# Optimization experiments

Measured on AMD Instinct MI355X. Metric: run time of the kernel, lower is better.

## Reference

```python
import jax, jax.numpy as jnp
import numpy as np

D_MODEL = 256
N_LAYERS = 6
N_HEADS = 8
D_FF = 1024
HEAD_DIM = D_MODEL // N_HEADS
EPS = 1e-5


def layer_norm(x, scale, bias):
    mu = jnp.mean(x, axis=-1, keepdims=True)
    var = jnp.var(x, axis=-1, keepdims=True)
    return (x - mu) * jax.lax.rsqrt(var + EPS) * scale + bias


def setup_inputs() -> dict:
    key = jax.random.key(0)
    ks = jax.random.split(key, 12)
    B, T = 4, 2048
    x = jax.random.normal(ks[0], (B, T, D_MODEL), dtype=jnp.float32)
    L = N_LAYERS
    s = 0.02
    inp = {
        "x": x,
        "ln1_s": jnp.ones((L, D_MODEL), jnp.float32),
        "ln1_b": jnp.zeros((L, D_MODEL), jnp.float32),
        "wq": jax.random.normal(ks[1], (L, D_MODEL, D_MODEL), jnp.float32) * s,
        "bq": jnp.zeros((L, D_MODEL), jnp.float32),
        "wk": jax.random.normal(ks[2], (L, D_MODEL, D_MODEL), jnp.float32) * s,
        "bk": jnp.zeros((L, D_MODEL), jnp.float32),
        "wv": jax.random.normal(ks[3], (L, D_MODEL, D_MODEL), jnp.float32) * s,
        "bv": jnp.zeros((L, D_MODEL), jnp.float32),
        "wo": jax.random.normal(ks[4], (L, D_MODEL, D_MODEL), jnp.float32) * s,
        "bo": jnp.zeros((L, D_MODEL), jnp.float32),
        "ln2_s": jnp.ones((L, D_MODEL), jnp.float32),
        "ln2_b": jnp.zeros((L, D_MODEL), jnp.float32),
        "w1": jax.random.normal(ks[5], (L, D_MODEL, D_FF), jnp.float32) * s,
        "b1": jnp.zeros((L, D_FF), jnp.float32),
        "w2": jax.random.normal(ks[6], (L, D_FF, D_MODEL), jnp.float32) * s,
        "b2": jnp.zeros((L, D_MODEL), jnp.float32),
    }
    return inp


def reference(x, ln1_s, ln1_b, wq, bq, wk, bk, wv, bv, wo, bo, ln2_s, ln2_b, w1, b1, w2, b2):
    B, T, D = x.shape
    scale = 1.0 / jnp.sqrt(jnp.float32(HEAD_DIM))
    for l in range(N_LAYERS):
        normed = layer_norm(x, ln1_s[l], ln1_b[l])
        q = (normed @ wq[l] + bq[l]).reshape(B, T, N_HEADS, HEAD_DIM)
        k = (normed @ wk[l] + bk[l]).reshape(B, T, N_HEADS, HEAD_DIM)
        v = (normed @ wv[l] + bv[l]).reshape(B, T, N_HEADS, HEAD_DIM)
        scores = jnp.einsum('bqhd,bkhd->bhqk', q, k) * scale  # [B,H,T,T]
        attn = jax.nn.softmax(scores, axis=-1)
        attn_out = jnp.einsum('bhqk,bkhd->bqhd', attn, v).reshape(B, T, D)
        x = x + attn_out @ wo[l] + bo[l]
        h = layer_norm(x, ln2_s[l], ln2_b[l])
        h = jax.nn.gelu(h @ w1[l] + b1[l], approximate=False)
        x = x + h @ w2[l] + b2[l]
    return x
```

## Files before the change

kernel.cpp:

```cpp
#include <hip/hip_runtime.h>
#include <math.h>

#define D_MODELC 256
#define N_LAYERSC 6
#define N_HEADSC 8
#define D_FFC 1024
#define HEAD_DIMC 32
#define B_SZ 4
#define T_SEQ 2048
#define M_ROWS 8192
#define QKV_N 768

typedef short bf16x8 __attribute__((ext_vector_type(8)));
typedef short bf16x4 __attribute__((ext_vector_type(4)));
typedef float f32x4  __attribute__((ext_vector_type(4)));
typedef unsigned u32x4 __attribute__((ext_vector_type(4)));
typedef unsigned short u16;

#define QSCALE 0.25503488f

__device__ __forceinline__ u16 f2bf(float x) {
    unsigned u = __builtin_bit_cast(unsigned, x);
    u += 0x7FFF + ((u >> 16) & 1);
    return (u16)(u >> 16);
}

__device__ __forceinline__ float bf2f(short x) {
    return __builtin_bit_cast(float, (unsigned)((u16)x) << 16);
}

__device__ __forceinline__ unsigned pack2bf(float a, float b) {
    return __builtin_amdgcn_perm(__builtin_bit_cast(unsigned, b),
                                 __builtin_bit_cast(unsigned, a), 0x07060302u);
}

__device__ __forceinline__ float fast_gelu(float x) {
    float y  = x * 0.70710678118654752f;
    float ay = __builtin_fabsf(y);
    float t  = __builtin_amdgcn_rcpf(1.0f + 0.3275911f * ay);
    float p  = t * (0.254829592f + t * (-0.284496736f + t * (1.421413741f
               + t * (-1.453152027f + t * 1.061405429f))));
    float e  = __builtin_amdgcn_exp2f(-ay * ay * 1.4426950408889634f);
    float er = 1.0f - p * e;
    er = y < 0.0f ? -er : er;
    return 0.5f * x * (1.0f + er);
}

__device__ __forceinline__ void transpose_tile(
    const float* __restrict__ src, u16* __restrict__ dst,
    int K, int N, int k0, int n0, float scale, float (*ts)[33])
{
    const int r = threadIdx.x >> 3, c4 = (threadIdx.x & 7) * 4;
    const float4 v = *(const float4*)(src + (size_t)(k0 + r) * N + n0 + c4);
    ts[r][c4 + 0] = v.x; ts[r][c4 + 1] = v.y;
    ts[r][c4 + 2] = v.z; ts[r][c4 + 3] = v.w;
    __syncthreads();
    bf16x4 o;
#pragma unroll
    for (int i = 0; i < 4; i++) o[i] = (short)f2bf(ts[c4 + i][r] * scale);
    *(bf16x4*)(dst + (size_t)(n0 + r) * K + k0 + c4) = o;
}

__global__ __launch_bounds__(256) void prep_all(
    const float* __restrict__ wq, const float* __restrict__ wk,
    const float* __restrict__ wv, const float* __restrict__ wo,
    const float* __restrict__ w1, const float* __restrict__ w2,
    const float* __restrict__ bq, const float* __restrict__ bk,
    const float* __restrict__ bv,
    u16* __restrict__ wqkv_t, u16* __restrict__ wo_t,
    u16* __restrict__ w1_t, u16* __restrict__ w2_t,
    float* __restrict__ qkvb,
    const float* __restrict__ x, const float* __restrict__ gamma,
    const float* __restrict__ beta, float* __restrict__ X,
    u16* __restrict__ Y)
{
    __shared__ float ts[32][33];
    const int bid = blockIdx.x;
    if (bid < 1152) {
        const int sec = bid / 384, t = bid % 384;
        const int z = t >> 6, rem = t & 63, ty = rem >> 3, tx = rem & 7;
        const float* src = sec == 0 ? wq : (sec == 1 ? wk : wv);
        transpose_tile(src + (size_t)z * 65536,
                       wqkv_t + (size_t)z * QKV_N * 256 + sec * 256 * 256,
                       256, 256, ty * 32, tx * 32,
                       sec == 0 ? QSCALE : 1.0f, ts);
    } else if (bid < 1536) {
        const int t = bid - 1152;
        const int z = t >> 6, rem = t & 63, ty = rem >> 3, tx = rem & 7;
        transpose_tile(wo + (size_t)z * 65536, wo_t + (size_t)z * 65536,
                       256, 256, ty * 32, tx * 32, 1.0f, ts);
    } else if (bid < 3072) {
        const int t = bid - 1536;
        const int z = t >> 8, rem = t & 255, ty = rem >> 5, tx = rem & 31;
        transpose_tile(w1 + (size_t)z * 262144, w1_t + (size_t)z * 262144,
                       256, D_FFC, ty * 32, tx * 32, 1.0f, ts);
    } else if (bid < 4608) {
        const int t = bid - 3072;
        const int z = t >> 8, rem = t & 255, ty = rem >> 3, tx = rem & 7;
        transpose_tile(w2 + (size_t)z * 262144, w2_t + (size_t)z * 262144,
                       D_FFC, 256, ty * 32, tx * 32, 1.0f, ts);
    } else if (bid < 4626) {
        const int i = (bid - 4608) * 256 + threadIdx.x;
        const int l = i / QKV_N, j = i % QKV_N;
        float v;
        if (j < 256)      v = bq[l * 256 + j] * QSCALE;
        else if (j < 512) v = bk[l * 256 + j - 256];
        else              v = bv[l * 256 + j - 512];
        qkvb[i] = v;
    } else {
        const int w = threadIdx.x >> 6, lane = threadIdx.x & 63;
        const int row = (bid - 4626) * 4 + w;
        const float4 v = *(const float4*)(x + (size_t)row * 256 + lane * 4);
        *(float4*)(X + (size_t)row * 256 + lane * 4) = v;
        float sum = v.x + v.y + v.z + v.w;
        float sq  = v.x * v.x + v.y * v.y + v.z * v.z + v.w * v.w;
#pragma unroll
        for (int off = 32; off > 0; off >>= 1) {
            sum += __shfl_xor(sum, off, 64);
            sq  += __shfl_xor(sq,  off, 64);
        }
        float mu  = sum * (1.0f / 256.0f);
        float var = sq * (1.0f / 256.0f) - mu * mu;
        float rr  = rsqrtf(var + 1e-5f);
        const float4 g  = *(const float4*)(gamma + lane * 4);
        const float4 bb = *(const float4*)(beta + lane * 4);
        bf16x4 o;
        o[0] = (short)f2bf((v.x - mu) * rr * g.x + bb.x);
        o[1] = (short)f2bf((v.y - mu) * rr * g.y + bb.y);
        o[2] = (short)f2bf((v.z - mu) * rr * g.z + bb.z);
        o[3] = (short)f2bf((v.w - mu) * rr * g.w + bb.w);
        *(bf16x4*)(Y + (size_t)row * 256 + lane * 4) = o;
    }
}

template <int EPI>
__global__ __launch_bounds__(256) void mfma_gemm(
    const u16* __restrict__ A, const u16* __restrict__ Bt,
    const float* __restrict__ bias, u16* __restrict__ Vout,
    void* __restrict__ Cout, int N, int K)
{
    __shared__ u16 As[128 * 64];
    __shared__ u16 Bs[128 * 64];
    const int tid = threadIdx.x, w = tid >> 6, lane = tid & 63;
    const int c = lane & 15, quad = lane >> 4;
    const int row0 = blockIdx.y * 128, col0 = blockIdx.x * 128;
    const int wr = w >> 1, wc = w & 1;

    int flv[4], rA[4], colA[4];
#pragma unroll
    for (int ci = 0; ci < 4; ci++) {
        flv[ci]  = (w * 4 + ci) * 1024 + lane * 16;
        rA[ci]   = flv[ci] >> 7;
        colA[ci] = (flv[ci] & 127) >> 1;
    }

    f32x4 acc[4][4] = {};
    bf16x8 pA[4], pB[4];
#pragma unroll
    for (int ci = 0; ci < 4; ci++) {
        pA[ci] = *(const bf16x8*)(A  + (size_t)(row0 + rA[ci]) * K + colA[ci]);
        pB[ci] = *(const bf16x8*)(Bt + (size_t)(col0 + rA[ci]) * K + colA[ci]);
    }

    for (int k0 = 0; k0 < K; k0 += 64) {
        __syncthreads();
#pragma unroll
        for (int ci = 0; ci < 4; ci++) {
            *(bf16x8*)((char*)As + flv[ci]) = pA[ci];
            *(bf16x8*)((char*)Bs + flv[ci]) = pB[ci];
        }
        __syncthreads();
        if (k0 + 64 < K) {
#pragma unroll
            for (int ci = 0; ci < 4; ci++) {
                pA[ci] = *(const bf16x8*)(A  + (size_t)(row0 + rA[ci]) * K + k0 + 64 + colA[ci]);
                pB[ci] = *(const bf16x8*)(Bt + (size_t)(col0 + rA[ci]) * K + k0 + 64 + colA[ci]);
            }
        }
#pragma unroll
        for (int kk = 0; kk < 2; kk++) {
            bf16x8 af[4], bfv[4];
#pragma unroll
            for (int i = 0; i < 4; i++)
                af[i] = *(const bf16x8*)&As[(wr * 64 + i * 16 + c) * 64 + kk * 32 + quad * 8];
#pragma unroll
            for (int j = 0; j < 4; j++)
                bfv[j] = *(const bf16x8*)&Bs[(wc * 64 + j * 16 + c) * 64 + kk * 32 + quad * 8];
#pragma unroll
            for (int i = 0; i < 4; i++)
#pragma unroll
                for (int j = 0; j < 4; j++)
                    acc[i][j] = __builtin_amdgcn_mfma_f32_16x16x32_bf16(
                        af[i], bfv[j], acc[i][j], 0, 0, 0);
        }
    }

    float bj[4];
#pragma unroll
    for (int j = 0; j < 4; j++) bj[j] = bias[col0 + wc * 64 + j * 16 + c];

    if (EPI == 3 && col0 >= 512) {
#pragma unroll
        for (int i = 0; i < 4; i++) {
            const int tok = row0 + wr * 64 + i * 16 + quad * 4;
#pragma unroll
            for (int j = 0; j < 4; j++) {
                const int dim = col0 - 512 + wc * 64 + j * 16 + c;
                bf16x4 o;
#pragma unroll
                for (int r = 0; r < 4; r++) o[r] = (short)f2bf(acc[i][j][r] + bj[j]);
                *(bf16x4*)&Vout[(size_t)dim * M_ROWS + tok] = o;
            }
        }
        return;
    }

#pragma unroll
    for (int i = 0; i < 4; i++) {
#pragma unroll
        for (int r = 0; r < 4; r++) {
            const int gr = row0 + wr * 64 + i * 16 + quad * 4 + r;
#pragma unroll
            for (int j = 0; j < 4; j++) {
                const int gc = col0 + wc * 64 + j * 16 + c;
                float v = acc[i][j][r] + bj[j];
                if (EPI == 2) v = fast_gelu(v);
                ((u16*)Cout)[(size_t)gr * N + gc] = f2bf(v);
            }
        }
    }
}

template <int DOLN, int MERGE>
__global__ __launch_bounds__(256) void gemm_ln(
    const u16* __restrict__ A, const u16* __restrict__ Ab,
    const float* __restrict__ Lmrg,
    const u16* __restrict__ Bt, const float* __restrict__ bias,
    const float* __restrict__ resid, float* __restrict__ Xout,
    const float* __restrict__ gamma, const float* __restrict__ beta,
    u16* __restrict__ Nout, int K)
{
    __shared__ u16 As[32 * 64];
    __shared__ u16 Bs[256 * 64];
    __shared__ float2 red[4][32];
    const int tid = threadIdx.x, w = tid >> 6, lane = tid & 63;
    const int c = lane & 15, quad = lane >> 4;
    const int row0 = blockIdx.x * 32;

    const int flA  = w * 1024 + lane * 16;
    const int rAa  = flA >> 7, colAa = (flA & 127) >> 1;
    int flB[8], rB[8], colB[8];
#pragma unroll
    for (int ci = 0; ci < 8; ci++) {
        flB[ci]  = (w * 8 + ci) * 1024 + lane * 16;
        rB[ci]   = flB[ci] >> 7;
        colB[ci] = (flB[ci] & 127) >> 1;
    }

    f32x4 acc[2][4] = {};

    auto loadA = [&](int gc) -> bf16x8 {
        const int row = row0 + rAa;
        if (MERGE) {
            const int head = gc >> 5;
            const float la = Lmrg[(size_t)row * 8 + head];
            const float lb = Lmrg[(size_t)M_ROWS * 8 + (size_t)row * 8 + head];
            const float inv = __builtin_amdgcn_rcpf(la + lb);
            bf16x8 a = *(const bf16x8*)(A  + (size_t)row * 256 + gc);
            bf16x8 b = *(const bf16x8*)(Ab + (size_t)row * 256 + gc);
            bf16x8 o;
#pragma unroll
            for (int j = 0; j < 8; j++)
                o[j] = (short)f2bf((bf2f(a[j]) + bf2f(b[j])) * inv);
            return o;
        }
        return *(const bf16x8*)(A + (size_t)row * K + gc);
    };

    bf16x8 pA = loadA(colAa);
    bf16x8 pB[8];
#pragma unroll
    for (int ci = 0; ci < 8; ci++)
        pB[ci] = *(const bf16x8*)(Bt + (size_t)rB[ci] * K + colB[ci]);

    for (int k0 = 0; k0 < K; k0 += 64) {
        __syncthreads();
        *(bf16x8*)((char*)As + flA) = pA;
#pragma unroll
        for (int ci = 0; ci < 8; ci++)
            *(bf16x8*)((char*)Bs + flB[ci]) = pB[ci];
        __syncthreads();
        if (k0 + 64 < K) {
            pA = loadA(k0 + 64 + colAa);
#pragma unroll
            for (int ci = 0; ci < 8; ci++)
                pB[ci] = *(const bf16x8*)(Bt + (size_t)rB[ci] * K + k0 + 64 + colB[ci]);
        }
#pragma unroll
        for (int kk = 0; kk < 2; kk++) {
            bf16x8 af[2], bfv[4];
#pragma unroll
            for (int i = 0; i < 2; i++)
                af[i] = *(const bf16x8*)&As[(i * 16 + c) * 64 + kk * 32 + quad * 8];
#pragma unroll
            for (int j = 0; j < 4; j++)
                bfv[j] = *(const bf16x8*)&Bs[(w * 64 + j * 16 + c) * 64 + kk * 32 + quad * 8];
#pragma unroll
            for (int i = 0; i < 2; i++)
#pragma unroll
                for (int j = 0; j < 4; j++)
                    acc[i][j] = __builtin_amdgcn_mfma_f32_16x16x32_bf16(
                        af[i], bfv[j], acc[i][j], 0, 0, 0);
        }
    }

    float bj[4];
#pragma unroll
    for (int j = 0; j < 4; j++) bj[j] = bias[w * 64 + j * 16 + c];
    float xv[2][4][4];
#pragma unroll
    for (int i = 0; i < 2; i++)
#pragma unroll
        for (int r = 0; r < 4; r++) {
            const int gr = row0 + i * 16 + quad * 4 + r;
#pragma unroll
            for (int j = 0; j < 4; j++) {
                const int gc = w * 64 + j * 16 + c;
                xv[i][j][r] = acc[i][j][r] + bj[j] + resid[(size_t)gr * 256 + gc];
            }
        }

    if (DOLN) {
        float sm[2][4], sp[2][4];
#pragma unroll
        for (int i = 0; i < 2; i++)
#pragma unroll
            for (int r = 0; r < 4; r++) {
                float s = 0.f, q = 0.f;
#pragma unroll
                for (int j = 0; j < 4; j++) { s += xv[i][j][r]; q += xv[i][j][r] * xv[i][j][r]; }
                sm[i][r] = s; sp[i][r] = q;
            }
#pragma unroll
        for (int off = 1; off < 16; off <<= 1)
#pragma unroll
            for (int i = 0; i < 2; i++)
#pragma unroll
                for (int r = 0; r < 4; r++) {
                    sm[i][r] += __shfl_xor(sm[i][r], off, 64);
                    sp[i][r] += __shfl_xor(sp[i][r], off, 64);
                }
        __syncthreads();
        if (c == 0) {
#pragma unroll
            for (int i = 0; i < 2; i++)
#pragma unroll
                for (int r = 0; r < 4; r++)
                    red[w][i * 16 + quad * 4 + r] = make_float2(sm[i][r], sp[i][r]);
        }
        __syncthreads();
#pragma unroll
        for (int i = 0; i < 2; i++)
#pragma unroll
            for (int r = 0; r < 4; r++) {
                const int row = i * 16 + quad * 4 + r;
                float2 t0 = red[0][row], t1 = red[1][row];
                float2 t2 = red[2][row], t3 = red[3][row];
                float S = (t0.x + t1.x) + (t2.x + t3.x);
                float Q = (t0.y + t1.y) + (t2.y + t3.y);
                float mu = S * (1.0f / 256.0f);
                float var = Q * (1.0f / 256.0f) - mu * mu;
                float rr = rsqrtf(var + 1e-5f);
                const int gr = row0 + row;
#pragma unroll
                for (int j = 0; j < 4; j++) {
                    const int gc = w * 64 + j * 16 + c;
                    float x = xv[i][j][r];
                    Xout[(size_t)gr * 256 + gc] = x;
                    Nout[(size_t)gr * 256 + gc] =
                        f2bf((x - mu) * rr * gamma[gc] + beta[gc]);
                }
            }
    } else {
#pragma unroll
        for (int i = 0; i < 2; i++)
#pragma unroll
            for (int r = 0; r < 4; r++) {
                const int gr = row0 + i * 16 + quad * 4 + r;
#pragma unroll
                for (int j = 0; j < 4; j++)
                    Xout[(size_t)gr * 256 + w * 64 + j * 16 + c] = xv[i][j][r];
            }
    }
}

__global__ __launch_bounds__(256) void attn_kernel(
    const u16* __restrict__ QKV, const u16* __restrict__ VT,
    u16* __restrict__ POa, u16* __restrict__ POb, float* __restrict__ Lp)
{
    const int h = blockIdx.y, b = blockIdx.z;
    const int half = blockIdx.x & 1;
    const int q0 = (blockIdx.x >> 1) * 128;
    const int tid = threadIdx.x, w = tid >> 6, lane = tid & 63;
    const int c = lane & 15, quad = lane >> 4;

    __shared__ u16 Kf[4096];
    __shared__ u16 Vf[4096];

    const u16* qp = QKV + (size_t)(b * T_SEQ + q0 + w * 32 + c) * QKV_N + h * 32 + quad * 8;
    bf16x8 aQ0 = *(const bf16x8*)qp;
    bf16x8 aQ1 = *(const bf16x8*)(qp + 16 * QKV_N);

    const bf16x8 bOnes = {0x3F80, 0x3F80, 0x3F80, 0x3F80,
                          0x3F80, 0x3F80, 0x3F80, 0x3F80};

    f32x4 O[2][2] = {};
    f32x4 Ol0 = {0.f, 0.f, 0.f, 0.f}, Ol1 = {0.f, 0.f, 0.f, 0.f};

    const u16* kgp = QKV + (size_t)(b * T_SEQ + w * 16 + c) * QKV_N + 256 + h * 32 + quad * 8;
    const u16* vgp = VT + ((size_t)h * 32 + (lane & 31)) * M_ROWS + b * T_SEQ
                     + (w * 2 + (lane >> 5)) * 8;
    u16* kfw = Kf + w * 512 + lane * 8;

    const int vd  = lane & 31, vdh = vd >> 4, vc = vd & 15, vhi = lane >> 5;
    const int vkh = w >> 1, vseg = w & 1;
    const int voff = ((((vkh * 2 + vdh) * 4 + 2 * vhi) * 16 + vc) * 8) + vseg * 4;

    const int kbeg = half * (T_SEQ / 2);
    const int kend = kbeg + T_SEQ / 2;

    bf16x8 gK0 = *(const bf16x8*)(kgp + (size_t)kbeg * QKV_N);
    bf16x8 gK1 = *(const bf16x8*)(kgp + (size_t)(kbeg + 64) * QKV_N);
    bf16x8 gV0 = *(const bf16x8*)(vgp + kbeg);
    bf16x8 gV1 = *(const bf16x8*)(vgp + kbeg + 64);

    for (int k0 = kbeg; k0 < kend; k0 += 128) {
        __syncthreads();
        *(bf16x8*)kfw          = gK0;
        *(bf16x8*)(kfw + 2048) = gK1;
        {
            bf16x4 l0v = __builtin_shufflevector(gV0, gV0, 0, 1, 2, 3);
            bf16x4 h0v = __builtin_shufflevector(gV0, gV0, 4, 5, 6, 7);
            bf16x4 l1v = __builtin_shufflevector(gV1, gV1, 0, 1, 2, 3);
            bf16x4 h1v = __builtin_shufflevector(gV1, gV1, 4, 5, 6, 7);
            *(bf16x4*)&Vf[voff]              = l0v;
            *(bf16x4*)&Vf[voff + 128]        = h0v;
            *(bf16x4*)&Vf[2048 + voff]       = l1v;
            *(bf16x4*)&Vf[2048 + voff + 128] = h1v;
        }
        __syncthreads();
        if (k0 + 128 < kend) {
            gK0 = *(const bf16x8*)(kgp + (size_t)(k0 + 128) * QKV_N);
            gK1 = *(const bf16x8*)(kgp + (size_t)(k0 + 192) * QKV_N);
            gV0 = *(const bf16x8*)(vgp + k0 + 128);
            gV1 = *(const bf16x8*)(vgp + k0 + 192);
        }

#pragma unroll
        for (int hf = 0; hf < 2; hf++) {
            const u16* Kb = Kf + hf * 2048;
            const u16* Vb = Vf + hf * 2048;

            unsigned pk0[4][2], pk1[4][2];
#pragma unroll
            for (int g = 0; g < 4; g++) {
                bf16x8 aK = *(const bf16x8*)&Kb[g * 512 + lane * 8];
                f32x4 S0 = __builtin_amdgcn_mfma_f32_16x16x32_bf16(
                    aK, aQ0, (f32x4){0.f, 0.f, 0.f, 0.f}, 0, 0, 0);
                f32x4 S1 = __builtin_amdgcn_mfma_f32_16x16x32_bf16(
                    aK, aQ1, (f32x4){0.f, 0.f, 0.f, 0.f}, 0, 0, 0);
                pk0[g][0] = pack2bf(__builtin_amdgcn_exp2f(S0[0]),
                                    __builtin_amdgcn_exp2f(S0[1]));
                pk0[g][1] = pack2bf(__builtin_amdgcn_exp2f(S0[2]),
                                    __builtin_amdgcn_exp2f(S0[3]));
                pk1[g][0] = pack2bf(__builtin_amdgcn_exp2f(S1[0]),
                                    __builtin_amdgcn_exp2f(S1[1]));
                pk1[g][1] = pack2bf(__builtin_amdgcn_exp2f(S1[2]),
                                    __builtin_amdgcn_exp2f(S1[3]));
            }

            __builtin_amdgcn_s_setprio(1);
#pragma unroll
            for (int kh = 0; kh < 2; kh++) {
                bf16x8 aP0 = __builtin_bit_cast(bf16x8,
                    (u32x4){pk0[2 * kh][0], pk0[2 * kh][1],
                            pk0[2 * kh + 1][0], pk0[2 * kh + 1][1]});
                bf16x8 aP1 = __builtin_bit_cast(bf16x8,
                    (u32x4){pk1[2 * kh][0], pk1[2 * kh][1],
                            pk1[2 * kh + 1][0], pk1[2 * kh + 1][1]});
                Ol0 = __builtin_amdgcn_mfma_f32_16x16x32_bf16(aP0, bOnes, Ol0, 0, 0, 0);
                Ol1 = __builtin_amdgcn_mfma_f32_16x16x32_bf16(aP1, bOnes, Ol1, 0, 0, 0);
#pragma unroll
                for (int dh = 0; dh < 2; dh++) {
                    bf16x8 bV = *(const bf16x8*)&Vb[((kh * 2 + dh) * 64 + lane) * 8];
                    O[0][dh] = __builtin_amdgcn_mfma_f32_16x16x32_bf16(aP0, bV, O[0][dh], 0, 0, 0);
                    O[1][dh] = __builtin_amdgcn_mfma_f32_16x16x32_bf16(aP1, bV, O[1][dh], 0, 0, 0);
                }
            }
            __builtin_amdgcn_s_setprio(0);
        }
    }

    u16* pb = (half ? POb : POa)
              + (size_t)(b * T_SEQ + q0 + w * 32) * 256 + h * 32;
    if (c == 0) {
        float* lb = Lp + (size_t)half * M_ROWS * 8
                    + (size_t)(b * T_SEQ + q0 + w * 32) * 8 + h;
#pragma unroll
        for (int r = 0; r < 4; r++) {
            lb[(size_t)(quad * 4 + r) * 8]      = Ol0[r];
            lb[(size_t)(16 + quad * 4 + r) * 8] = Ol1[r];
        }
    }
#pragma unroll
    for (int r = 0; r < 4; r++) {
        int src = quad * 4 + r;
        pb[(size_t)src * 256 + c]             = f2bf(O[0][0][r]);
        pb[(size_t)src * 256 + 16 + c]        = f2bf(O[0][1][r]);
        pb[(size_t)(16 + src) * 256 + c]      = f2bf(O[1][0][r]);
        pb[(size_t)(16 + src) * 256 + 16 + c] = f2bf(O[1][1][r]);
    }
}

extern "C" void kernel_launch(void* const* d_in, const int* in_sizes, int n_in,
                              void* d_out, int out_size, void* d_ws, size_t ws_size,
                              hipStream_t stream)
{
    const float* x     = (const float*)d_in[0];
    const float* ln1_s = (const float*)d_in[1];
    const float* ln1_b = (const float*)d_in[2];
    const float* wq    = (const float*)d_in[3];
    const float* bq    = (const float*)d_in[4];
    const float* wk    = (const float*)d_in[5];
    const float* bk    = (const float*)d_in[6];
    const float* wv    = (const float*)d_in[7];
    const float* bv    = (const float*)d_in[8];
    const float* wo    = (const float*)d_in[9];
    const float* bo    = (const float*)d_in[10];
    const float* ln2_s = (const float*)d_in[11];
    const float* ln2_b = (const float*)d_in[12];
    const float* w1    = (const float*)d_in[13];
    const float* b1    = (const float*)d_in[14];
    const float* w2    = (const float*)d_in[15];
    const float* b2    = (const float*)d_in[16];

    float* X = (float*)d_out;

    u16* normed = (u16*)d_ws;
    u16* qkv    = normed + (size_t)M_ROWS * 256;
    u16* POa    = qkv + (size_t)M_ROWS * QKV_N;
    u16* h1     = qkv;
    u16* wqkv_t = POa + (size_t)M_ROWS * 256;
    u16* wo_t   = wqkv_t + (size_t)N_LAYERSC * QKV_N * 256;
    u16* w1_t   = wo_t + (size_t)N_LAYERSC * 256 * 256;
    u16* w2_t   = w1_t + (size_t)N_LAYERSC * D_FFC * 256;
    float* qkvb = (float*)(w2_t + (size_t)N_LAYERSC * 256 * D_FFC);
    u16* VTb    = (u16*)(qkvb + N_LAYERSC * QKV_N);
    u16* POb    = VTb + (size_t)256 * M_ROWS;
    float* Lp   = (float*)(POb + (size_t)M_ROWS * 256);

    dim3 blk(256);

    prep_all<<<dim3(4626 + M_ROWS / 4), blk, 0, stream>>>(
        wq, wk, wv, wo, w1, w2, bq, bk, bv,
        wqkv_t, wo_t, w1_t, w2_t, qkvb,
        x, ln1_s, ln1_b, X, normed);

    dim3 g_qkv(QKV_N / 128, M_ROWS / 128);
    dim3 g_ff(D_FFC / 128, M_ROWS / 128);
    dim3 g_ln32(M_ROWS / 32);
    dim3 g_attn(2 * T_SEQ / 128, N_HEADSC, B_SZ);

    for (int l = 0; l < N_LAYERSC; l++) {
        mfma_gemm<3><<<g_qkv, blk, 0, stream>>>(
            normed, wqkv_t + (size_t)l * QKV_N * 256, qkvb + l * QKV_N,
            VTb, qkv, QKV_N, 256);
        attn_kernel<<<g_attn, blk, 0, stream>>>(qkv, VTb, POa, POb, Lp);
        gemm_ln<1, 1><<<g_ln32, blk, 0, stream>>>(
            POa, POb, Lp, wo_t + (size_t)l * 256 * 256, bo + l * 256, X,
            X, ln2_s + l * 256, ln2_b + l * 256, VTb, 256);
        mfma_gemm<2><<<g_ff, blk, 0, stream>>>(
            VTb, w1_t + (size_t)l * D_FFC * 256, b1 + l * D_FFC,
            nullptr, h1, D_FFC, 256);
        if (l + 1 < N_LAYERSC) {
            gemm_ln<1, 0><<<g_ln32, blk, 0, stream>>>(
                h1, nullptr, nullptr, w2_t + (size_t)l * 256 * D_FFC,
                b2 + l * 256, X, X, ln1_s + (l + 1) * 256,
                ln1_b + (l + 1) * 256, normed, D_FFC);
        } else {
            gemm_ln<0, 0><<<g_ln32, blk, 0, stream>>>(
                h1, nullptr, nullptr, w2_t + (size_t)l * 256 * D_FFC,
                b2 + l * 256, X, X, nullptr, nullptr, nullptr, D_FFC);
        }
    }
}
```

Baseline: 618.1 us.

## Fuse all layers into one persistent cooperative megakernel with grid barriers

```diff
diff --git a/kernel.cpp b/kernel.cpp
--- a/kernel.cpp
+++ b/kernel.cpp
@@ -5,11 +5,11 @@
 #define N_LAYERSC 6
 #define N_HEADSC 8
 #define D_FFC 1024
-#define HEAD_DIMC 32
 #define B_SZ 4
 #define T_SEQ 2048
 #define M_ROWS 8192
 #define QKV_N 768
+#define NBLK_MAX 512
 
 typedef short bf16x8 __attribute__((ext_vector_type(8)));
 typedef short bf16x4 __attribute__((ext_vector_type(4)));
@@ -46,6 +46,19 @@
     return 0.5f * x * (1.0f + er);
 }
 
+__device__ __forceinline__ void gsync(unsigned* bar, unsigned& epoch) {
+    __syncthreads();
+    epoch += gridDim.x;
+    if (threadIdx.x == 0) {
+        __threadfence();
+        __hip_atomic_fetch_add(bar, 1u, __ATOMIC_ACQ_REL, __HIP_MEMORY_SCOPE_AGENT);
+        while (__hip_atomic_load(bar, __ATOMIC_RELAXED, __HIP_MEMORY_SCOPE_AGENT) < epoch)
+            __builtin_amdgcn_s_sleep(2);
+        __threadfence();
+    }
+    __syncthreads();
+}
+
 __device__ __forceinline__ void transpose_tile(
     const float* __restrict__ src, u16* __restrict__ dst,
     int K, int N, int k0, int n0, float scale, float (*ts)[33])
@@ -61,7 +74,8 @@
     *(bf16x4*)(dst + (size_t)(n0 + r) * K + k0 + c4) = o;
 }
 
-__global__ __launch_bounds__(256) void prep_all(
+__device__ __forceinline__ void prep_tile(
+    int bid,
     const float* __restrict__ wq, const float* __restrict__ wk,
     const float* __restrict__ wv, const float* __restrict__ wo,
     const float* __restrict__ w1, const float* __restrict__ w2,
@@ -72,10 +86,9 @@
     float* __restrict__ qkvb,
     const float* __restrict__ x, const float* __restrict__ gamma,
     const float* __restrict__ beta, float* __restrict__ X,
-    u16* __restrict__ Y)
+    u16* __restrict__ Y, char* smem)
 {
-    __shared__ float ts[32][33];
-    const int bid = blockIdx.x;
+    float (*ts)[33] = (float(*)[33])smem;
     if (bid < 1152) {
         const int sec = bid / 384, t = bid % 384;
         const int z = t >> 6, rem = t & 63, ty = rem >> 3, tx = rem & 7;
@@ -133,17 +146,17 @@
     }
 }
 
-template <int EPI>
-__global__ __launch_bounds__(256) void mfma_gemm(
+__device__ __forceinline__ void gemm128_tile(
     const u16* __restrict__ A, const u16* __restrict__ Bt,
     const float* __restrict__ bias, u16* __restrict__ Vout,
-    void* __restrict__ Cout, int N, int K)
+    u16* __restrict__ Cout, int N, int K, int bx, int by,
+    bool qkvmode, bool gelu, char* smem)
 {
-    __shared__ u16 As[128 * 64];
-    __shared__ u16 Bs[128 * 64];
+    u16* As = (u16*)smem;
+    u16* Bs = (u16*)(smem + 16384);
     const int tid = threadIdx.x, w = tid >> 6, lane = tid & 63;
     const int c = lane & 15, quad = lane >> 4;
-    const int row0 = blockIdx.y * 128, col0 = blockIdx.x * 128;
+    const int row0 = by * 128, col0 = bx * 128;
     const int wr = w >> 1, wc = w & 1;
 
     int flv[4], rA[4], colA[4];
@@ -199,7 +212,7 @@
 #pragma unroll
     for (int j = 0; j < 4; j++) bj[j] = bias[col0 + wc * 64 + j * 16 + c];
 
-    if (EPI == 3 && col0 >= 512) {
+    if (qkvmode && col0 >= 512) {
 #pragma unroll
         for (int i = 0; i < 4; i++) {
             const int tok = row0 + wr * 64 + i * 16 + quad * 4;
@@ -224,28 +237,26 @@
             for (int j = 0; j < 4; j++) {
                 const int gc = col0 + wc * 64 + j * 16 + c;
                 float v = acc[i][j][r] + bj[j];
-                if (EPI == 2) v = fast_gelu(v);
-                ((u16*)Cout)[(size_t)gr * N + gc] = f2bf(v);
-            }
-        }
-    }
-}
-
-template <int DOLN, int MERGE>
-__global__ __launch_bounds__(256) void gemm_ln(
-    const u16* __restrict__ A, const u16* __restrict__ Ab,
-    const float* __restrict__ Lmrg,
-    const u16* __restrict__ Bt, const float* __restrict__ bias,
-    const float* __restrict__ resid, float* __restrict__ Xout,
-    const float* __restrict__ gamma, const float* __restrict__ beta,
-    u16* __restrict__ Nout, int K)
+                if (gelu) v = fast_gelu(v);
+                Cout[(size_t)gr * N + gc] = f2bf(v);
+            }
+        }
+    }
+}
+
+__device__ __forceinline__ void gemmln_tile(
+    const u16* __restrict__ A, const u16* __restrict__ Bt,
+    const float* __restrict__ bias, const float* __restrict__ resid,
+    float* __restrict__ Xout, const float* __restrict__ gamma,
+    const float* __restrict__ beta, u16* __restrict__ Nout,
+    int K, bool doln, int tix, char* smem)
 {
-    __shared__ u16 As[32 * 64];
-    __shared__ u16 Bs[256 * 64];
-    __shared__ float2 red[4][32];
+    u16* As = (u16*)smem;
+    u16* Bs = (u16*)(smem + 4096);
+    float2 (*red)[32] = (float2(*)[32])(smem + 36864);
     const int tid = threadIdx.x, w = tid >> 6, lane = tid & 63;
     const int c = lane & 15, quad = lane >> 4;
-    const int row0 = blockIdx.x * 32;
+    const int row0 = tix * 32;
 
     const int flA  = w * 1024 + lane * 16;
     const int rAa  = flA >> 7, colAa = (flA & 127) >> 1;
@@ -259,25 +270,7 @@
 
     f32x4 acc[2][4] = {};
 
-    auto loadA = [&](int gc) -> bf16x8 {
-        const int row = row0 + rAa;
-        if (MERGE) {
-            const int head = gc >> 5;
-            const float la = Lmrg[(size_t)row * 8 + head];
-            const float lb = Lmrg[(size_t)M_ROWS * 8 + (size_t)row * 8 + head];
-            const float inv = __builtin_amdgcn_rcpf(la + lb);
-            bf16x8 a = *(const bf16x8*)(A  + (size_t)row * 256 + gc);
-            bf16x8 b = *(const bf16x8*)(Ab + (size_t)row * 256 + gc);
-            bf16x8 o;
-#pragma unroll
-            for (int j = 0; j < 8; j++)
-                o[j] = (short)f2bf((bf2f(a[j]) + bf2f(b[j])) * inv);
-            return o;
-        }
-        return *(const bf16x8*)(A + (size_t)row * K + gc);
-    };
-
-    bf16x8 pA = loadA(colAa);
+    bf16x8 pA = *(const bf16x8*)(A + (size_t)(row0 + rAa) * K + colAa);
     bf16x8 pB[8];
 #pragma unroll
     for (int ci = 0; ci < 8; ci++)
@@ -291,7 +284,7 @@
             *(bf16x8*)((char*)Bs + flB[ci]) = pB[ci];
         __syncthreads();
         if (k0 + 64 < K) {
-            pA = loadA(k0 + 64 + colAa);
+            pA = *(const bf16x8*)(A + (size_t)(row0 + rAa) * K + k0 + 64 + colAa);
 #pragma unroll
             for (int ci = 0; ci < 8; ci++)
                 pB[ci] = *(const bf16x8*)(Bt + (size_t)rB[ci] * K + k0 + 64 + colB[ci]);
@@ -330,7 +323,7 @@
             }
         }
 
-    if (DOLN) {
+    if (doln) {
         float sm[2][4], sp[2][4];
 #pragma unroll
         for (int i = 0; i < 2; i++)
@@ -375,10 +368,10 @@
 #pragma unroll
                 for (int j = 0; j < 4; j++) {
                     const int gc = w * 64 + j * 16 + c;
-                    float x = xv[i][j][r];
-                    Xout[(size_t)gr * 256 + gc] = x;
+                    float xx = xv[i][j][r];
+                    Xout[(size_t)gr * 256 + gc] = xx;
                     Nout[(size_t)gr * 256 + gc] =
-                        f2bf((x - mu) * rr * gamma[gc] + beta[gc]);
+                        f2bf((xx - mu) * rr * gamma[gc] + beta[gc]);
                 }
             }
     } else {
@@ -394,18 +387,16 @@
     }
 }
 
-__global__ __launch_bounds__(256) void attn_kernel(
+__device__ __forceinline__ void attn_tile(
     const u16* __restrict__ QKV, const u16* __restrict__ VT,
-    u16* __restrict__ POa, u16* __restrict__ POb, float* __restrict__ Lp)
+    u16* __restrict__ PO, int tix, char* smem)
 {
-    const int h = blockIdx.y, b = blockIdx.z;
-    const int half = blockIdx.x & 1;
-    const int q0 = (blockIdx.x >> 1) * 128;
+    u16* Kf = (u16*)smem;
+    u16* Vf = (u16*)(smem + 8192);
+    const int b = tix >> 7, h = (tix >> 4) & 7;
+    const int q0 = (tix & 15) * 128;
     const int tid = threadIdx.x, w = tid >> 6, lane = tid & 63;
     const int c = lane & 15, quad = lane >> 4;
-
-    __shared__ u16 Kf[4096];
-    __shared__ u16 Vf[4096];
 
     const u16* qp = QKV + (size_t)(b * T_SEQ + q0 + w * 32 + c) * QKV_N + h * 32 + quad * 8;
     bf16x8 aQ0 = *(const bf16x8*)qp;
@@ -426,15 +417,12 @@
     const int vkh = w >> 1, vseg = w & 1;
     const int voff = ((((vkh * 2 + vdh) * 4 + 2 * vhi) * 16 + vc) * 8) + vseg * 4;
 
-    const int kbeg = half * (T_SEQ / 2);
-    const int kend = kbeg + T_SEQ / 2;
-
-    bf16x8 gK0 = *(const bf16x8*)(kgp + (size_t)kbeg * QKV_N);
-    bf16x8 gK1 = *(const bf16x8*)(kgp + (size_t)(kbeg + 64) * QKV_N);
-    bf16x8 gV0 = *(const bf16x8*)(vgp + kbeg);
-    bf16x8 gV1 = *(const bf16x8*)(vgp + kbeg + 64);
-
-    for (int k0 = kbeg; k0 < kend; k0 += 128) {
+    bf16x8 gK0 = *(const bf16x8*)(kgp);
+    bf16x8 gK1 = *(const bf16x8*)(kgp + (size_t)64 * QKV_N);
+    bf16x8 gV0 = *(const bf16x8*)(vgp);
+    bf16x8 gV1 = *(const bf16x8*)(vgp + 64);
+
+    for (int k0 = 0; k0 < T_SEQ; k0 += 128) {
         __syncthreads();
         *(bf16x8*)kfw          = gK0;
         *(bf16x8*)(kfw + 2048) = gK1;
@@ -449,7 +437,7 @@
             *(bf16x4*)&Vf[2048 + voff + 128] = h1v;
         }
         __syncthreads();
-        if (k0 + 128 < kend) {
+        if (k0 + 128 < T_SEQ) {
             gK0 = *(const bf16x8*)(kgp + (size_t)(k0 + 128) * QKV_N);
             gK1 = *(const bf16x8*)(kgp + (size_t)(k0 + 192) * QKV_N);
             gV0 = *(const bf16x8*)(vgp + k0 + 128);
@@ -501,24 +489,81 @@
         }
     }
 
-    u16* pb = (half ? POb : POa)
-              + (size_t)(b * T_SEQ + q0 + w * 32) * 256 + h * 32;
-    if (c == 0) {
-        float* lb = Lp + (size_t)half * M_ROWS * 8
-                    + (size_t)(b * T_SEQ + q0 + w * 32) * 8 + h;
-#pragma unroll
-        for (int r = 0; r < 4; r++) {
-            lb[(size_t)(quad * 4 + r) * 8]      = Ol0[r];
-            lb[(size_t)(16 + quad * 4 + r) * 8] = Ol1[r];
-        }
+    u16* pb = PO + (size_t)(b * T_SEQ + q0 + w * 32) * 256 + h * 32;
+    f32x4 r0, r1;
+#pragma unroll
+    for (int r = 0; r < 4; r++) {
+        r0[r] = __builtin_amdgcn_rcpf(Ol0[r]);
+        r1[r] = __builtin_amdgcn_rcpf(Ol1[r]);
     }
 #pragma unroll
     for (int r = 0; r < 4; r++) {
         int src = quad * 4 + r;
-        pb[(size_t)src * 256 + c]             = f2bf(O[0][0][r]);
-        pb[(size_t)src * 256 + 16 + c]        = f2bf(O[0][1][r]);
-        pb[(size_t)(16 + src) * 256 + c]      = f2bf(O[1][0][r]);
-        pb[(size_t)(16 + src) * 256 + 16 + c] = f2bf(O[1][1][r]);
+        pb[(size_t)src * 256 + c]             = f2bf(O[0][0][r] * r0[r]);
+        pb[(size_t)src * 256 + 16 + c]        = f2bf(O[0][1][r] * r0[r]);
+        pb[(size_t)(16 + src) * 256 + c]      = f2bf(O[1][0][r] * r1[r]);
+        pb[(size_t)(16 + src) * 256 + 16 + c] = f2bf(O[1][1][r] * r1[r]);
+    }
+}
+
+__global__ __launch_bounds__(256, 2) void mega_transformer(
+    const float* __restrict__ wq, const float* __restrict__ wk,
+    const float* __restrict__ wv, const float* __restrict__ wo,
+    const float* __restrict__ w1, const float* __restrict__ w2,
+    const float* __restrict__ bq, const float* __restrict__ bk,
+    const float* __restrict__ bv, const float* __restrict__ bo,
+    const float* __restrict__ b1, const float* __restrict__ b2,
+    const float* __restrict__ ln1_s, const float* __restrict__ ln1_b,
+    const float* __restrict__ ln2_s, const float* __restrict__ ln2_b,
+    const float* __restrict__ x,
+    float* __restrict__ X, u16* __restrict__ normed, u16* __restrict__ qkv,
+    u16* __restrict__ PO, u16* __restrict__ wqkv_t, u16* __restrict__ wo_t,
+    u16* __restrict__ w1_t, u16* __restrict__ w2_t, float* __restrict__ qkvb,
+    u16* __restrict__ VTb, unsigned* __restrict__ bar)
+{
+    __shared__ __align__(16) char smem[37888];
+    unsigned epoch = 0;
+    const int bid = blockIdx.x;
+    const int nblk = gridDim.x;
+
+    for (int t = bid; t < 6674; t += nblk) {
+        __syncthreads();
+        prep_tile(t, wq, wk, wv, wo, w1, w2, bq, bk, bv,
+                  wqkv_t, wo_t, w1_t, w2_t, qkvb,
+                  x, ln1_s, ln1_b, X, normed, smem);
+    }
+    gsync(bar, epoch);
+
+    u16* h1 = qkv;
+
+    for (int l = 0; l < N_LAYERSC; l++) {
+        for (int t = bid; t < 384; t += nblk)
+            gemm128_tile(normed, wqkv_t + (size_t)l * QKV_N * 256,
+                         qkvb + l * QKV_N, VTb, qkv,
+                         QKV_N, 256, t % 6, t / 6, true, false, smem);
+        gsync(bar, epoch);
+
+        for (int t = bid; t < 512; t += nblk)
+            attn_tile(qkv, VTb, PO, t, smem);
+        gsync(bar, epoch);
+
+        for (int t = bid; t < 256; t += nblk)
+            gemmln_tile(PO, wo_t + (size_t)l * 65536, bo + l * 256, X, X,
+                        ln2_s + l * 256, ln2_b + l * 256, VTb, 256, true, t, smem);
+        gsync(bar, epoch);
+
+        for (int t = bid; t < 512; t += nblk)
+            gemm128_tile(VTb, w1_t + (size_t)l * D_FFC * 256, b1 + l * D_FFC,
+                         nullptr, h1, D_FFC, 256, t & 7, t >> 3, false, true, smem);
+        gsync(bar, epoch);
+
+        const bool dol = (l + 1 < N_LAYERSC);
+        const int ln = dol ? l + 1 : 0;
+        for (int t = bid; t < 256; t += nblk)
+            gemmln_tile(h1, w2_t + (size_t)l * 256 * D_FFC, b2 + l * 256, X, X,
+                        ln1_s + ln * 256, ln1_b + ln * 256, normed,
+                        D_FFC, dol, t, smem);
+        if (l + 1 < N_LAYERSC) gsync(bar, epoch);
     }
 }
 
@@ -548,49 +593,39 @@
 
     u16* normed = (u16*)d_ws;
     u16* qkv    = normed + (size_t)M_ROWS * 256;
-    u16* POa    = qkv + (size_t)M_ROWS * QKV_N;
-    u16* h1     = qkv;
-    u16* wqkv_t = POa + (size_t)M_ROWS * 256;
+    u16* PO     = qkv + (size_t)M_ROWS * QKV_N;
+    u16* wqkv_t = PO + (size_t)M_ROWS * 256;
     u16* wo_t   = wqkv_t + (size_t)N_LAYERSC * QKV_N * 256;
     u16* w1_t   = wo_t + (size_t)N_LAYERSC * 256 * 256;
     u16* w2_t   = w1_t + (size_t)N_LAYERSC * D_FFC * 256;
     float* qkvb = (float*)(w2_t + (size_t)N_LAYERSC * 256 * D_FFC);
     u16* VTb    = (u16*)(qkvb + N_LAYERSC * QKV_N);
-    u16* POb    = VTb + (size_t)256 * M_ROWS;
-    float* Lp   = (float*)(POb + (size_t)M_ROWS * 256);
-
-    dim3 blk(256);
-
-    prep_all<<<dim3(4626 + M_ROWS / 4), blk, 0, stream>>>(
-        wq, wk, wv, wo, w1, w2, bq, bk, bv,
-        wqkv_t, wo_t, w1_t, w2_t, qkvb,
-        x, ln1_s, ln1_b, X, normed);
-
-    dim3 g_qkv(QKV_N / 128, M_ROWS / 128);
-    dim3 g_ff(D_FFC / 128, M_ROWS / 128);
-    dim3 g_ln32(M_ROWS / 32);
-    dim3 g_attn(2 * T_SEQ / 128, N_HEADSC, B_SZ);
-
-    for (int l = 0; l < N_LAYERSC; l++) {
-        mfma_gemm<3><<<g_qkv, blk, 0, stream>>>(
-            normed, wqkv_t + (size_t)l * QKV_N * 256, qkvb + l * QKV_N,
-            VTb, qkv, QKV_N, 256);
-        attn_kernel<<<g_attn, blk, 0, stream>>>(qkv, VTb, POa, POb, Lp);
-        gemm_ln<1, 1><<<g_ln32, blk, 0, stream>>>(
-            POa, POb, Lp, wo_t + (size_t)l * 256 * 256, bo + l * 256, X,
-            X, ln2_s + l * 256, ln2_b + l * 256, VTb, 256);
-        mfma_gemm<2><<<g_ff, blk, 0, stream>>>(
-            VTb, w1_t + (size_t)l * D_FFC * 256, b1 + l * D_FFC,
-            nullptr, h1, D_FFC, 256);
-        if (l + 1 < N_LAYERSC) {
-            gemm_ln<1, 0><<<g_ln32, blk, 0, stream>>>(
-                h1, nullptr, nullptr, w2_t + (size_t)l * 256 * D_FFC,
-                b2 + l * 256, X, X, ln1_s + (l + 1) * 256,
-                ln1_b + (l + 1) * 256, normed, D_FFC);
-        } else {
-            gemm_ln<0, 0><<<g_ln32, blk, 0, stream>>>(
-                h1, nullptr, nullptr, w2_t + (size_t)l * 256 * D_FFC,
-                b2 + l * 256, X, X, nullptr, nullptr, nullptr, D_FFC);
-        }
-    }
-}
+    unsigned* bar = (unsigned*)((char*)d_ws + (64u << 20));
+
+    hipMemsetAsync(bar, 0, 256, stream);
+
+    int maxb = 0;
+    if (hipOccupancyMaxActiveBlocksPerMultiprocessor(&maxb, mega_transformer, 256, 0)
+            != hipSuccess || maxb < 1)
+        maxb = 1;
+    int nblk = maxb * 256;
+    if (nblk > NBLK_MAX) nblk = NBLK_MAX;
+
+    void* kargs[] = {
+        (void*)&wq, (void*)&wk, (void*)&wv, (void*)&wo, (void*)&w1, (void*)&w2,
+        (void*)&bq, (void*)&bk, (void*)&bv, (void*)&bo, (void*)&b1, (void*)&b2,
+        (void*)&ln1_s, (void*)&ln1_b, (void*)&ln2_s, (void*)&ln2_b, (void*)&x,
+        (void*)&X, (void*)&normed, (void*)&qkv, (void*)&PO, (void*)&wqkv_t,
+        (void*)&wo_t, (void*)&w1_t, (void*)&w2_t, (void*)&qkvb, (void*)&VTb,
+        (void*)&bar
+    };
+
+    hipError_t err = hipLaunchCooperativeKernel(
+        mega_transformer, dim3(nblk), dim3(256), kargs, 0, stream);
+    if (err != hipSuccess) {
+        mega_transformer<<<dim3(nblk), dim3(256), 0, stream>>>(
+            wq, wk, wv, wo, w1, w2, bq, bk, bv, bo, b1, b2,
+            ln1_s, ln1_b, ln2_s, ln2_b, x,
+            X, normed, qkv, PO, wqkv_t, wo_t, w1_t, w2_t, qkvb, VTb, bar);
+    }
+}
```

New measurement: 1.673 ms. 2.71x slower.
